# Kernel optimization log

Measured on AMD Instinct MI355X. Metric: run time of the kernel, lower is better.

## Reference

```python
import jax, jax.numpy as jnp
import numpy as np

N = 50000
E = 400000
NFEAT = 256
NHID = 64
HEADS = [4, 4, 4]
NCLASS = 121
NEG_SLOPE = 0.2


def gat_conv(h, W, al, ar, src, dst, H, D):
    # h: [N, F_in], W: [F_in, H*D], al/ar: [H, D]
    feat = (h @ W).reshape(N, H, D)                    # [N, H, D]
    el = jnp.sum(feat * al[None], axis=-1)             # [N, H]
    er = jnp.sum(feat * ar[None], axis=-1)             # [N, H]
    e = jax.nn.leaky_relu(el[src] + er[dst], NEG_SLOPE)  # [E, H]
    # edge softmax over incoming edges of each dst node
    m = jax.ops.segment_max(e, dst, num_segments=N)    # [N, H]
    ex = jnp.exp(e - m[dst])                           # [E, H]
    s = jax.ops.segment_sum(ex, dst, num_segments=N)   # [N, H]
    alpha = ex / s[dst]                                # [E, H]
    msg = alpha[..., None] * feat[src]                 # [E, H, D]
    return jax.ops.segment_sum(msg, dst, num_segments=N)  # [N, H, D]


def setup_inputs() -> dict:
    key = jax.random.key(0)
    ks = jax.random.split(key, 12)
    d = {
        "h": jax.random.normal(ks[0], (N, NFEAT), dtype=jnp.float32),
        "src": jax.random.randint(ks[1], (E,), 0, N),
        "dst": jax.random.randint(ks[2], (E,), 0, N),
        "W1": jax.random.normal(ks[3], (NFEAT, HEADS[0] * NHID), dtype=jnp.float32) * 0.05,
        "al1": jax.random.normal(ks[4], (HEADS[0], NHID), dtype=jnp.float32) * 0.1,
        "ar1": jax.random.normal(ks[5], (HEADS[0], NHID), dtype=jnp.float32) * 0.1,
        "W2": jax.random.normal(ks[6], (HEADS[0] * NHID, HEADS[1] * NHID), dtype=jnp.float32) * 0.05,
        "al2": jax.random.normal(ks[7], (HEADS[1], NHID), dtype=jnp.float32) * 0.1,
        "ar2": jax.random.normal(ks[8], (HEADS[1], NHID), dtype=jnp.float32) * 0.1,
        "W3": jax.random.normal(ks[9], (HEADS[1] * NHID, HEADS[2] * NCLASS), dtype=jnp.float32) * 0.05,
        "al3": jax.random.normal(ks[10], (HEADS[2], NCLASS), dtype=jnp.float32) * 0.1,
        "ar3": jax.random.normal(ks[11], (HEADS[2], NCLASS), dtype=jnp.float32) * 0.1,
    }
    return d


def reference(h, src, dst, W1, al1, ar1, W2, al2, ar2, W3, al3, ar3):
    # layer 1: [N, H0, NHID] -> flatten -> ELU (norm='none', drop=0, residual='none')
    x = gat_conv(h, W1, al1, ar1, src, dst, HEADS[0], NHID).reshape(N, -1)
    x = jax.nn.elu(x)
    # layer 2
    x = gat_conv(x, W2, al2, ar2, src, dst, HEADS[1], NHID).reshape(N, -1)
    x = jax.nn.elu(x)
    # output layer: mean over heads
    x = gat_conv(x, W3, al3, ar3, src, dst, HEADS[2], NCLASS).mean(axis=1)
    return x
```

## Files before the change

kernel.cpp:

```cpp
#include <hip/hip_runtime.h>
#include <cstddef>

#define NN 50000
#define NE 400000
#define NH 4
#define NC 121
#define MAXSLOT 600000

typedef __attribute__((ext_vector_type(8))) short short8;
typedef __attribute__((ext_vector_type(4))) float f32x4;
typedef __attribute__((ext_vector_type(2))) float f32x2;

static __device__ __forceinline__ unsigned short f2bf(float f) {
    unsigned u = __float_as_uint(f);
    u += 0x7fffu + ((u >> 16) & 1u);
    return (unsigned short)(u >> 16);
}
static __device__ __forceinline__ f32x2 bfpair(unsigned u) {
    f32x2 r;
    r.x = __uint_as_float(u << 16);
    r.y = __uint_as_float(u & 0xffff0000u);
    return r;
}
static __device__ __forceinline__ void load_lds16(const unsigned short* g, unsigned short* l) {
    __builtin_amdgcn_global_load_lds(
        (const __attribute__((address_space(1))) unsigned*)g,
        (__attribute__((address_space(3))) unsigned*)l, 16, 0, 0);
}

#define PREP_X    3200000
#define PREP_BT1  (PREP_X + 65536)
#define PREP_BT2  (PREP_BT1 + 65536)
#define PREP_CAT  (PREP_BT2 + 131072)
#define PREP_WV   (PREP_CAT + 2048)
#define PREP_SENT (PREP_WV + 256)
#define PREP_END  (PREP_SENT + NE)
__global__ __launch_bounds__(256) void prep_k(const float* __restrict__ h,
                                              const float* __restrict__ W1,
                                              const float* __restrict__ W2,
                                              const float* __restrict__ W3,
                                              const float* __restrict__ al3,
                                              const float* __restrict__ ar3,
                                              const int* __restrict__ dst,
                                              unsigned short* __restrict__ h_bf,
                                              unsigned short* __restrict__ BT1,
                                              unsigned short* __restrict__ BT2,
                                              unsigned short* __restrict__ BTcat,
                                              float* __restrict__ wl3,
                                              float* __restrict__ wr3,
                                              unsigned short* __restrict__ feat_bf,
                                              float* __restrict__ el,
                                              int* __restrict__ deg) {
    int i = blockIdx.x * blockDim.x + threadIdx.x;
    if (i < PREP_X) {
        float4 v = *(const float4*)&h[(size_t)i * 4];
        ushort4 o;
        o.x = f2bf(v.x); o.y = f2bf(v.y); o.z = f2bf(v.z); o.w = f2bf(v.w);
        *(ushort4*)&h_bf[(size_t)i * 4] = o;
    } else if (i < PREP_BT1) {
        int j = i - PREP_X;
        int n = j >> 8, k = j & 255;
        BT1[j] = f2bf(W1[(size_t)k * 256 + n]);
    } else if (i < PREP_BT2) {
        int j = i - PREP_BT1;
        int n = j >> 8, k = j & 255;
        BT2[j] = f2bf(W2[(size_t)k * 256 + n]);
    } else if (i < PREP_CAT) {
        int j = i - PREP_BT2;
        int c = j >> 10, kk = j & 1023;
        int hh = kk >> 8, k = kk & 255;
        float v = (c < NC) ? 0.25f * W3[(size_t)k * 484 + hh * NC + c] : 0.f;
        BTcat[j] = f2bf(v);
    } else if (i < PREP_WV) {
        int j = (i - PREP_CAT) & 1023;
        int sel = (i - PREP_CAT) >> 10;
        int hh = j >> 8, k = j & 255;
        const float* a = sel ? ar3 : al3;
        const float* wrow = W3 + (size_t)k * 484 + hh * NC;
        const float* arow = a + hh * NC;
        float s = 0.f;
        for (int d = 0; d < NC; ++d) s += wrow[d] * arow[d];
        if (sel) wr3[j] = s; else wl3[j] = s;
    } else if (i < PREP_SENT) {
        int j = i - PREP_WV;
        feat_bf[(size_t)NN * 256 + j] = 0;
        if (j < 4) el[NN * 4 + j] = -1e30f;
    } else if (i < PREP_END) {
        atomicAdd(&deg[dst[i - PREP_SENT]], 1);
    }
}

__global__ __launch_bounds__(512) void gemm256(const unsigned short* __restrict__ A,
                                               const unsigned short* __restrict__ BT,
                                               unsigned short* __restrict__ Cb,
                                               const float* __restrict__ al,
                                               const float* __restrict__ ar,
                                               float* __restrict__ el,
                                               float* __restrict__ er,
                                               int M) {
    const int K = 256;
    __shared__ __align__(16) unsigned short Alds[128 * 32];
    __shared__ __align__(16) unsigned short Blds[256 * 32];
    const int tid = threadIdx.x;
    const int wave = tid >> 6;
    const int lane = tid & 63;
    const int quad = lane >> 4;
    const int ml = lane & 15;
    const int m0 = blockIdx.x * 128;
    const int wm0 = (wave >> 2) * 64;
    const int wn0 = (wave & 3) * 64;

    const unsigned short* Ab = A + (size_t)(m0 + wave * 16 + (lane >> 2)) * K + (lane & 3) * 8;
    const unsigned short* Bb = BT + (size_t)(wave * 16 + (lane >> 2)) * K + (lane & 3) * 8;
    unsigned short* AldsW = Alds + wave * 512;
    unsigned short* BldsW = Blds + wave * 512;

    f32x4 acc[4][4] = {};

    for (int k0 = 0; k0 < K; k0 += 32) {
        load_lds16(Ab + k0, AldsW);
        #pragma unroll
        for (int p = 0; p < 2; ++p)
            load_lds16(Bb + (size_t)(p * 128) * K + k0, BldsW + p * 4096);
        __syncthreads();

        short8 af[4], bf[4];
        #pragma unroll
        for (int i = 0; i < 4; ++i)
            af[i] = *(const short8*)&Alds[(wm0 + i * 16 + ml) * 32 + quad * 8];
        #pragma unroll
        for (int j = 0; j < 4; ++j)
            bf[j] = *(const short8*)&Blds[(wn0 + j * 16 + ml) * 32 + quad * 8];
        #pragma unroll
        for (int i = 0; i < 4; ++i)
            #pragma unroll
            for (int j = 0; j < 4; ++j)
                acc[i][j] = __builtin_amdgcn_mfma_f32_16x16x32_bf16(af[i], bf[j], acc[i][j], 0, 0, 0);
        __syncthreads();
    }

    #pragma unroll
    for (int i = 0; i < 4; ++i) {
        #pragma unroll
        for (int reg = 0; reg < 4; ++reg) {
            int m = m0 + wm0 + i * 16 + quad * 4 + reg;
            if (m >= M) continue;
            #pragma unroll
            for (int j = 0; j < 4; ++j) {
                int n = wn0 + j * 16 + ml;
                Cb[(size_t)m * 256 + n] = f2bf(acc[i][j][reg]);
            }
        }
    }

    {
        int head = wave & 3;
        float alv[4], arv[4];
        #pragma unroll
        for (int j = 0; j < 4; ++j) {
            alv[j] = al[head * 64 + j * 16 + ml];
            arv[j] = ar[head * 64 + j * 16 + ml];
        }
        #pragma unroll
        for (int i = 0; i < 4; ++i) {
            #pragma unroll
            for (int reg = 0; reg < 4; ++reg) {
                float sl = 0.f, sr = 0.f;
                #pragma unroll
                for (int j = 0; j < 4; ++j) {
                    float v = acc[i][j][reg];
                    sl += v * alv[j];
                    sr += v * arv[j];
                }
                #pragma unroll
                for (int off = 1; off < 16; off <<= 1) {
                    sl += __shfl_xor(sl, off);
                    sr += __shfl_xor(sr, off);
                }
                int m = m0 + wm0 + i * 16 + quad * 4 + reg;
                if (ml == 0 && m < M) {
                    el[m * 4 + head] = sl;
                    er[m * 4 + head] = sr;
                }
            }
        }
    }
}

__global__ __launch_bounds__(256) void gemm_bf16(const unsigned short* __restrict__ A,
                                                 const unsigned short* __restrict__ BT,
                                                 float* __restrict__ Cf,
                                                 int M, int Nout, int K) {
    __shared__ __align__(16) unsigned short Alds[128 * 32];
    __shared__ __align__(16) unsigned short Blds[128 * 32];
    const int tid = threadIdx.x;
    const int wave = tid >> 6;
    const int lane = tid & 63;
    const int quad = lane >> 4;
    const int ml = lane & 15;
    const int m0 = blockIdx.x * 128;
    const int n0 = blockIdx.y * 128;
    const int wm0 = (wave >> 1) * 64;
    const int wn0 = (wave & 1) * 64;

    const unsigned short* Ab = A + (size_t)(m0 + wave * 16 + (lane >> 2)) * K + (lane & 3) * 8;
    const unsigned short* Bb = BT + (size_t)(n0 + wave * 16 + (lane >> 2)) * K + (lane & 3) * 8;
    unsigned short* AldsW = Alds + wave * 512;
    unsigned short* BldsW = Blds + wave * 512;

    f32x4 acc[4][4] = {};

    for (int k0 = 0; k0 < K; k0 += 32) {
        #pragma unroll
        for (int p = 0; p < 2; ++p) {
            load_lds16(Ab + (size_t)(p * 64) * K + k0, AldsW + p * 2048);
            load_lds16(Bb + (size_t)(p * 64) * K + k0, BldsW + p * 2048);
        }
        __syncthreads();

        short8 af[4], bf[4];
        #pragma unroll
        for (int i = 0; i < 4; ++i)
            af[i] = *(const short8*)&Alds[(wm0 + i * 16 + ml) * 32 + quad * 8];
        #pragma unroll
        for (int j = 0; j < 4; ++j)
            bf[j] = *(const short8*)&Blds[(wn0 + j * 16 + ml) * 32 + quad * 8];
        #pragma unroll
        for (int i = 0; i < 4; ++i)
            #pragma unroll
            for (int j = 0; j < 4; ++j)
                acc[i][j] = __builtin_amdgcn_mfma_f32_16x16x32_bf16(af[i], bf[j], acc[i][j], 0, 0, 0);
        __syncthreads();
    }

    #pragma unroll
    for (int i = 0; i < 4; ++i) {
        #pragma unroll
        for (int reg = 0; reg < 4; ++reg) {
            int m = m0 + wm0 + i * 16 + quad * 4 + reg;
            if (m >= M) continue;
            #pragma unroll
            for (int j = 0; j < 4; ++j) {
                int n = n0 + wn0 + j * 16 + ml;
                if (n < Nout) Cf[(size_t)m * Nout + n] = acc[i][j][reg];
            }
        }
    }
}

__global__ __launch_bounds__(256) void rowptr_k(const int* __restrict__ deg,
                                                int* __restrict__ rowptr,
                                                int* __restrict__ gtotal,
                                                int* __restrict__ ssrc,
                                                int* __restrict__ sdst) {
    __shared__ int sh[256];
    __shared__ int base;
    int i = blockIdx.x * 256 + threadIdx.x;
    int d = (i < NN) ? deg[i] : 0;
    int v = (d + 3) & ~3;
    sh[threadIdx.x] = v;
    __syncthreads();
    for (int off = 1; off < 256; off <<= 1) {
        int t = (threadIdx.x >= off) ? sh[threadIdx.x - off] : 0;
        __syncthreads();
        sh[threadIdx.x] += t;
        __syncthreads();
    }
    if (threadIdx.x == 255) base = atomicAdd(gtotal, sh[255]);
    __syncthreads();
    if (i < NN) {
        int rp = base + sh[threadIdx.x] - v;
        rowptr[i] = rp;
        for (int p = d; p < v; ++p) {
            ssrc[rp + p] = NN << 9;
            sdst[rp + p] = -1;
        }
    }
}

__global__ __launch_bounds__(256) void scatter_k(const int* __restrict__ src,
                                                 const int* __restrict__ dst,
                                                 const int* __restrict__ rowptr,
                                                 int* __restrict__ cursor,
                                                 int* __restrict__ ssrc,
                                                 int* __restrict__ sdst) {
    int e = blockIdx.x * blockDim.x + threadIdx.x;
    if (e >= NE) return;
    int d = dst[e];
    int p = atomicAdd(&cursor[d], 1);
    int pos = rowptr[d] + p;
    ssrc[pos] = src[e] << 9;
    sdst[pos] = d;
}

__global__ __launch_bounds__(256) void edgew_k(const int* __restrict__ ssrc,
                                               const int* __restrict__ sdst,
                                               const int* __restrict__ gtotal,
                                               const float* __restrict__ el,
                                               const float* __restrict__ er,
                                               float* __restrict__ wcsr) {
    int i = blockIdx.x * blockDim.x + threadIdx.x;
    if (i >= gtotal[0]) return;
    int d = sdst[i];
    float w0 = 0.f, w1 = 0.f, w2 = 0.f, w3 = 0.f;
    if (d >= 0) {
        int su = ssrc[i];
        float4 e_l = *(const float4*)((const char*)el + (su >> 5));
        float4 e_r = *(const float4*)&er[d * 4];
        float v0 = e_l.x + e_r.x; v0 = fmaxf(v0, 0.2f * v0);
        float v1 = e_l.y + e_r.y; v1 = fmaxf(v1, 0.2f * v1);
        float v2 = e_l.z + e_r.z; v2 = fmaxf(v2, 0.2f * v2);
        float v3 = e_l.w + e_r.w; v3 = fmaxf(v3, 0.2f * v3);
        w0 = __expf(v0); w1 = __expf(v1); w2 = __expf(v2); w3 = __expf(v3);
    }
    wcsr[0 * MAXSLOT + i] = w0;
    wcsr[1 * MAXSLOT + i] = w1;
    wcsr[2 * MAXSLOT + i] = w2;
    wcsr[3 * MAXSLOT + i] = w3;
}

__global__ __launch_bounds__(256) void agg256(const int* __restrict__ rowptr,
                                              const int* __restrict__ deg,
                                              const int* __restrict__ ssrc,
                                              const float* __restrict__ el,
                                              const float* __restrict__ er,
                                              const unsigned short* __restrict__ feat,
                                              unsigned short* __restrict__ ybf,
                                              const float* __restrict__ wl3,
                                              const float* __restrict__ wr3,
                                              float* __restrict__ el3,
                                              float* __restrict__ er3) {
    int wid = (blockIdx.x * blockDim.x + threadIdx.x) >> 6;
    int lane = threadIdx.x & 63;
    if (wid >= NN) return;
    int n = wid;
    int start = rowptr[n];
    int cnt4 = (deg[n] + 3) & ~3;
    int head = lane >> 4;
    float ern = er[n * 4 + head];
    const char* elb = (const char*)el + head * 4;
    const char* fbase = (const char*)feat + lane * 8;
    f32x2 a01 = {0.f, 0.f}, a23 = {0.f, 0.f};
    float ssum = 0.f;
    for (int k = 0; k < cnt4; k += 4) {
        int4 sv = *(const int4*)&ssrc[start + k];
        float e0 = *(const float*)(elb + (sv.x >> 5));
        float e1 = *(const float*)(elb + (sv.y >> 5));
        float e2 = *(const float*)(elb + (sv.z >> 5));
        float e3 = *(const float*)(elb + (sv.w >> 5));
        float v0 = e0 + ern; v0 = fmaxf(v0, 0.2f * v0); float w0 = __expf(v0);
        float v1 = e1 + ern; v1 = fmaxf(v1, 0.2f * v1); float w1 = __expf(v1);
        float v2 = e2 + ern; v2 = fmaxf(v2, 0.2f * v2); float w2 = __expf(v2);
        float v3 = e3 + ern; v3 = fmaxf(v3, 0.2f * v3); float w3 = __expf(v3);
        uint2 u0 = *(const uint2*)(fbase + sv.x);
        uint2 u1 = *(const uint2*)(fbase + sv.y);
        uint2 u2 = *(const uint2*)(fbase + sv.z);
        uint2 u3 = *(const uint2*)(fbase + sv.w);
        ssum += (w0 + w1) + (w2 + w3);
        a01 += w0 * bfpair(u0.x); a23 += w0 * bfpair(u0.y);
        a01 += w1 * bfpair(u1.x); a23 += w1 * bfpair(u1.y);
        a01 += w2 * bfpair(u2.x); a23 += w2 * bfpair(u2.y);
        a01 += w3 * bfpair(u3.x); a23 += w3 * bfpair(u3.y);
    }
    float inv = ssum > 0.f ? 1.0f / ssum : 0.f;
    float r0 = a01.x * inv, r1 = a01.y * inv, r2 = a23.x * inv, r3 = a23.y * inv;
    r0 = r0 > 0.f ? r0 : (__expf(r0) - 1.f);
    r1 = r1 > 0.f ? r1 : (__expf(r1) - 1.f);
    r2 = r2 > 0.f ? r2 : (__expf(r2) - 1.f);
    r3 = r3 > 0.f ? r3 : (__expf(r3) - 1.f);
    ushort4 o;
    o.x = f2bf(r0); o.y = f2bf(r1); o.z = f2bf(r2); o.w = f2bf(r3);
    *(ushort4*)&ybf[(size_t)n * 256 + lane * 4] = o;

    if (wl3) {
        float sl[4], sr[4];
        #pragma unroll
        for (int h = 0; h < 4; ++h) {
            float4 a4 = *(const float4*)&wl3[h * 256 + lane * 4];
            float4 b4 = *(const float4*)&wr3[h * 256 + lane * 4];
            sl[h] = r0 * a4.x + r1 * a4.y + r2 * a4.z + r3 * a4.w;
            sr[h] = r0 * b4.x + r1 * b4.y + r2 * b4.z + r3 * b4.w;
        }
        #pragma unroll
        for (int off = 32; off; off >>= 1) {
            #pragma unroll
            for (int h = 0; h < 4; ++h) {
                sl[h] += __shfl_xor(sl[h], off);
                sr[h] += __shfl_xor(sr[h], off);
            }
        }
        if (lane == 0) {
            #pragma unroll
            for (int h = 0; h < 4; ++h) {
                el3[n * 4 + h] = sl[h];
                er3[n * 4 + h] = sr[h];
            }
        }
    }
}

__global__ __launch_bounds__(256) void agg3(const int* __restrict__ rowptr,
                                            const int* __restrict__ deg,
                                            const int* __restrict__ ssrc,
                                            const float* __restrict__ wcsr,
                                            const unsigned short* __restrict__ x,
                                            unsigned short* __restrict__ xagg) {
    int wid = (blockIdx.x * blockDim.x + threadIdx.x) >> 6;
    int lane = threadIdx.x & 63;
    if (wid >= NN) return;
    int n = wid;
    int start = rowptr[n];
    int cnt4 = (deg[n] + 3) & ~3;
    const char* xbase = (const char*)x + lane * 8;
    f32x2 accA[4] = {}, accB[4] = {};
    float ssum[4] = {};
    for (int k = 0; k < cnt4; k += 4) {
        int4 sv = *(const int4*)&ssrc[start + k];
        float4 w0 = *(const float4*)&wcsr[0 * MAXSLOT + start + k];
        float4 w1 = *(const float4*)&wcsr[1 * MAXSLOT + start + k];
        float4 w2 = *(const float4*)&wcsr[2 * MAXSLOT + start + k];
        float4 w3 = *(const float4*)&wcsr[3 * MAXSLOT + start + k];
        uint2 u0 = *(const uint2*)(xbase + sv.x);
        uint2 u1 = *(const uint2*)(xbase + sv.y);
        uint2 u2 = *(const uint2*)(xbase + sv.z);
        uint2 u3 = *(const uint2*)(xbase + sv.w);
        ssum[0] += (w0.x + w0.y) + (w0.z + w0.w);
        ssum[1] += (w1.x + w1.y) + (w1.z + w1.w);
        ssum[2] += (w2.x + w2.y) + (w2.z + w2.w);
        ssum[3] += (w3.x + w3.y) + (w3.z + w3.w);
        f32x2 fa = bfpair(u0.x), fA = bfpair(u0.y);
        f32x2 fb = bfpair(u1.x), fB = bfpair(u1.y);
        f32x2 fc = bfpair(u2.x), fC = bfpair(u2.y);
        f32x2 fd = bfpair(u3.x), fD = bfpair(u3.y);
        accA[0] += w0.x * fa + w0.y * fb + w0.z * fc + w0.w * fd;
        accB[0] += w0.x * fA + w0.y * fB + w0.z * fC + w0.w * fD;
        accA[1] += w1.x * fa + w1.y * fb + w1.z * fc + w1.w * fd;
        accB[1] += w1.x * fA + w1.y * fB + w1.z * fC + w1.w * fD;
        accA[2] += w2.x * fa + w2.y * fb + w2.z * fc + w2.w * fd;
        accB[2] += w2.x * fA + w2.y * fB + w2.z * fC + w2.w * fD;
        accA[3] += w3.x * fa + w3.y * fb + w3.z * fc + w3.w * fd;
        accB[3] += w3.x * fA + w3.y * fB + w3.z * fC + w3.w * fD;
    }
    #pragma unroll
    for (int h = 0; h < 4; ++h) {
        float inv = ssum[h] > 0.f ? 1.f / ssum[h] : 0.f;
        ushort4 o;
        o.x = f2bf(accA[h].x * inv); o.y = f2bf(accA[h].y * inv);
        o.z = f2bf(accB[h].x * inv); o.w = f2bf(accB[h].y * inv);
        *(ushort4*)&xagg[(size_t)n * 1024 + h * 256 + lane * 4] = o;
    }
}

extern "C" void kernel_launch(void* const* d_in, const int* in_sizes, int n_in,
                              void* d_out, int out_size, void* d_ws, size_t ws_size,
                              hipStream_t stream) {
    const float* h   = (const float*)d_in[0];
    const int*   src = (const int*)d_in[1];
    const int*   dst = (const int*)d_in[2];
    const float* W1  = (const float*)d_in[3];
    const float* al1 = (const float*)d_in[4];
    const float* ar1 = (const float*)d_in[5];
    const float* W2  = (const float*)d_in[6];
    const float* al2 = (const float*)d_in[7];
    const float* ar2 = (const float*)d_in[8];
    const float* W3  = (const float*)d_in[9];
    const float* al3 = (const float*)d_in[10];
    const float* ar3 = (const float*)d_in[11];
    float* out = (float*)d_out;

    float* ws = (float*)d_ws;
    unsigned short* x_bf    = (unsigned short*)ws;
    unsigned short* h_bf    = (unsigned short*)(ws + 6400000);
    unsigned short* feat_bf = (unsigned short*)(ws + 12800000);
    unsigned short* xagg    = (unsigned short*)(ws + 6400000);
    float* el  = ws + 32000000;
    float* er  = ws + 32200064;
    float* wl3 = ws + 32400064;
    float* wr3 = ws + 32401088;
    unsigned short* BT1   = (unsigned short*)(ws + 32402112);
    unsigned short* BT2   = (unsigned short*)(ws + 32434880);
    unsigned short* BTcat = (unsigned short*)(ws + 32467648);
    float* wcsr = ws + 32533184;
    int* ibase  = (int*)(ws + 34933184);
    int* deg      = ibase;
    int* cursor   = ibase + 50000;
    int* gtotal   = ibase + 100000;
    int* rowptr   = ibase + 100256;
    int* ssrc     = ibase + 150256;
    int* sdst     = ibase + 750256;
    float* el2 = ws + 36283440;
    float* er2 = ws + 36483440;

    const int NB = (NN + 255) / 256;
    const int SLOT_BLOCKS = (MAXSLOT + 255) / 256;

    hipMemsetAsync(deg, 0, (2 * NN + 1) * sizeof(int), stream);

    prep_k<<<(PREP_END + 255) / 256, 256, 0, stream>>>(h, W1, W2, W3, al3, ar3, dst,
                                                       h_bf, BT1, BT2, BTcat, wl3, wr3,
                                                       feat_bf, el, deg);

    rowptr_k<<<NB, 256, 0, stream>>>(deg, rowptr, gtotal, ssrc, sdst);
    scatter_k<<<(NE + 255) / 256, 256, 0, stream>>>(src, dst, rowptr, cursor, ssrc, sdst);

    const int GB = (NN + 127) / 128;
    const int WAVE_BLOCKS = (NN * 64 + 255) / 256;

    gemm256<<<GB, 512, 0, stream>>>(h_bf, BT1, feat_bf, al1, ar1, el, er, NN);
    agg256<<<WAVE_BLOCKS, 256, 0, stream>>>(rowptr, deg, ssrc, el, er, feat_bf, x_bf,
                                            nullptr, nullptr, nullptr, nullptr);

    gemm256<<<GB, 512, 0, stream>>>(x_bf, BT2, feat_bf, al2, ar2, el, er, NN);
    agg256<<<WAVE_BLOCKS, 256, 0, stream>>>(rowptr, deg, ssrc, el, er, feat_bf, x_bf,
                                            wl3, wr3, el2, er2);

    edgew_k<<<SLOT_BLOCKS, 256, 0, stream>>>(ssrc, sdst, gtotal, el2, er2, wcsr);
    agg3<<<WAVE_BLOCKS, 256, 0, stream>>>(rowptr, deg, ssrc, wcsr, x_bf, xagg);
    gemm_bf16<<<dim3(GB, 1), 256, 0, stream>>>(xagg, BTcat, out, NN, NC, 1024);
}
```

Baseline: 376.1 us.

## Fuse layer-3 edge weight computation into agg3 via lane-parallel exp and shuffles

Removes the separate edgew_k kernel and the wcsr buffer, along with the sdst array used only to feed it. agg3 now has each lane compute the exp-leaky-relu weight for one incoming edge, using the el2 row of the source and the er2 row of the destination, then broadcasts the weights across the wave with __shfl. This drops one kernel launch and the global write and read-back of the four-head edge weight arrays, plus the sdst writes in rowptr and scatter. In exchange agg3 does more shuffle and ALU work per edge, and el2 padding is now set to -1e30 so padded slots get a weight of zero.

```diff
diff --git a/kernel.cpp b/kernel.cpp
--- a/kernel.cpp
+++ b/kernel.cpp
@@ -5,7 +5,6 @@
 #define NE 400000
 #define NH 4
 #define NC 121
-#define MAXSLOT 600000
 
 typedef __attribute__((ext_vector_type(8))) short short8;
 typedef __attribute__((ext_vector_type(4))) float f32x4;
@@ -50,6 +49,7 @@
                                               float* __restrict__ wr3,
                                               unsigned short* __restrict__ feat_bf,
                                               float* __restrict__ el,
+                                              float* __restrict__ el2,
                                               int* __restrict__ deg) {
     int i = blockIdx.x * blockDim.x + threadIdx.x;
     if (i < PREP_X) {
@@ -84,7 +84,10 @@
     } else if (i < PREP_SENT) {
         int j = i - PREP_WV;
         feat_bf[(size_t)NN * 256 + j] = 0;
-        if (j < 4) el[NN * 4 + j] = -1e30f;
+        if (j < 4) {
+            el[NN * 4 + j]  = -1e30f;
+            el2[NN * 4 + j] = -1e30f;
+        }
     } else if (i < PREP_END) {
         atomicAdd(&deg[dst[i - PREP_SENT]], 1);
     }
@@ -251,8 +254,7 @@
 __global__ __launch_bounds__(256) void rowptr_k(const int* __restrict__ deg,
                                                 int* __restrict__ rowptr,
                                                 int* __restrict__ gtotal,
-                                                int* __restrict__ ssrc,
-                                                int* __restrict__ sdst) {
+                                                int* __restrict__ ssrc) {
     __shared__ int sh[256];
     __shared__ int base;
     int i = blockIdx.x * 256 + threadIdx.x;
@@ -271,10 +273,8 @@
     if (i < NN) {
         int rp = base + sh[threadIdx.x] - v;
         rowptr[i] = rp;
-        for (int p = d; p < v; ++p) {
+        for (int p = d; p < v; ++p)
             ssrc[rp + p] = NN << 9;
-            sdst[rp + p] = -1;
-        }
     }
 }
 
@@ -282,41 +282,12 @@
                                                  const int* __restrict__ dst,
                                                  const int* __restrict__ rowptr,
                                                  int* __restrict__ cursor,
-                                                 int* __restrict__ ssrc,
-                                                 int* __restrict__ sdst) {
+                                                 int* __restrict__ ssrc) {
     int e = blockIdx.x * blockDim.x + threadIdx.x;
     if (e >= NE) return;
     int d = dst[e];
     int p = atomicAdd(&cursor[d], 1);
-    int pos = rowptr[d] + p;
-    ssrc[pos] = src[e] << 9;
-    sdst[pos] = d;
-}
-
-__global__ __launch_bounds__(256) void edgew_k(const int* __restrict__ ssrc,
-                                               const int* __restrict__ sdst,
-                                               const int* __restrict__ gtotal,
-                                               const float* __restrict__ el,
-                                               const float* __restrict__ er,
-                                               float* __restrict__ wcsr) {
-    int i = blockIdx.x * blockDim.x + threadIdx.x;
-    if (i >= gtotal[0]) return;
-    int d = sdst[i];
-    float w0 = 0.f, w1 = 0.f, w2 = 0.f, w3 = 0.f;
-    if (d >= 0) {
-        int su = ssrc[i];
-        float4 e_l = *(const float4*)((const char*)el + (su >> 5));
-        float4 e_r = *(const float4*)&er[d * 4];
-        float v0 = e_l.x + e_r.x; v0 = fmaxf(v0, 0.2f * v0);
-        float v1 = e_l.y + e_r.y; v1 = fmaxf(v1, 0.2f * v1);
-        float v2 = e_l.z + e_r.z; v2 = fmaxf(v2, 0.2f * v2);
-        float v3 = e_l.w + e_r.w; v3 = fmaxf(v3, 0.2f * v3);
-        w0 = __expf(v0); w1 = __expf(v1); w2 = __expf(v2); w3 = __expf(v3);
-    }
-    wcsr[0 * MAXSLOT + i] = w0;
-    wcsr[1 * MAXSLOT + i] = w1;
-    wcsr[2 * MAXSLOT + i] = w2;
-    wcsr[3 * MAXSLOT + i] = w3;
+    ssrc[rowptr[d] + p] = src[e] << 9;
 }
 
 __global__ __launch_bounds__(256) void agg256(const int* __restrict__ rowptr,
@@ -402,7 +373,8 @@
 __global__ __launch_bounds__(256) void agg3(const int* __restrict__ rowptr,
                                             const int* __restrict__ deg,
                                             const int* __restrict__ ssrc,
-                                            const float* __restrict__ wcsr,
+                                            const float* __restrict__ el,
+                                            const float* __restrict__ er,
                                             const unsigned short* __restrict__ x,
                                             unsigned short* __restrict__ xagg) {
     int wid = (blockIdx.x * blockDim.x + threadIdx.x) >> 6;
@@ -412,34 +384,54 @@
     int start = rowptr[n];
     int cnt4 = (deg[n] + 3) & ~3;
     const char* xbase = (const char*)x + lane * 8;
+    float4 ern = *(const float4*)&er[n * 4];
     f32x2 accA[4] = {}, accB[4] = {};
     float ssum[4] = {};
-    for (int k = 0; k < cnt4; k += 4) {
-        int4 sv = *(const int4*)&ssrc[start + k];
-        float4 w0 = *(const float4*)&wcsr[0 * MAXSLOT + start + k];
-        float4 w1 = *(const float4*)&wcsr[1 * MAXSLOT + start + k];
-        float4 w2 = *(const float4*)&wcsr[2 * MAXSLOT + start + k];
-        float4 w3 = *(const float4*)&wcsr[3 * MAXSLOT + start + k];
-        uint2 u0 = *(const uint2*)(xbase + sv.x);
-        uint2 u1 = *(const uint2*)(xbase + sv.y);
-        uint2 u2 = *(const uint2*)(xbase + sv.z);
-        uint2 u3 = *(const uint2*)(xbase + sv.w);
-        ssum[0] += (w0.x + w0.y) + (w0.z + w0.w);
-        ssum[1] += (w1.x + w1.y) + (w1.z + w1.w);
-        ssum[2] += (w2.x + w2.y) + (w2.z + w2.w);
-        ssum[3] += (w3.x + w3.y) + (w3.z + w3.w);
-        f32x2 fa = bfpair(u0.x), fA = bfpair(u0.y);
-        f32x2 fb = bfpair(u1.x), fB = bfpair(u1.y);
-        f32x2 fc = bfpair(u2.x), fC = bfpair(u2.y);
-        f32x2 fd = bfpair(u3.x), fD = bfpair(u3.y);
-        accA[0] += w0.x * fa + w0.y * fb + w0.z * fc + w0.w * fd;
-        accB[0] += w0.x * fA + w0.y * fB + w0.z * fC + w0.w * fD;
-        accA[1] += w1.x * fa + w1.y * fb + w1.z * fc + w1.w * fd;
-        accB[1] += w1.x * fA + w1.y * fB + w1.z * fC + w1.w * fD;
-        accA[2] += w2.x * fa + w2.y * fb + w2.z * fc + w2.w * fd;
-        accB[2] += w2.x * fA + w2.y * fB + w2.z * fC + w2.w * fD;
-        accA[3] += w3.x * fa + w3.y * fb + w3.z * fc + w3.w * fd;
-        accB[3] += w3.x * fA + w3.y * fB + w3.z * fC + w3.w * fD;
+    for (int base = 0; base < cnt4; base += 64) {
+        float4 w4 = {0.f, 0.f, 0.f, 0.f};
+        int idx = base + lane;
+        if (idx < cnt4) {
+            int su = ssrc[start + idx];
+            float4 e4 = *(const float4*)((const char*)el + (su >> 5));
+            float v0 = e4.x + ern.x; v0 = fmaxf(v0, 0.2f * v0); w4.x = __expf(v0);
+            float v1 = e4.y + ern.y; v1 = fmaxf(v1, 0.2f * v1); w4.y = __expf(v1);
+            float v2 = e4.z + ern.z; v2 = fmaxf(v2, 0.2f * v2); w4.z = __expf(v2);
+            float v3 = e4.w + ern.w; v3 = fmaxf(v3, 0.2f * v3); w4.w = __expf(v3);
+        }
+        int rem = cnt4 - base;
+        int kend = rem > 64 ? 64 : rem;
+        for (int k = 0; k < kend; k += 4) {
+            int4 sv = *(const int4*)&ssrc[start + base + k];
+            float4 wE0, wE1, wE2, wE3;
+            wE0.x = __shfl(w4.x, k);     wE0.y = __shfl(w4.y, k);
+            wE0.z = __shfl(w4.z, k);     wE0.w = __shfl(w4.w, k);
+            wE1.x = __shfl(w4.x, k + 1); wE1.y = __shfl(w4.y, k + 1);
+            wE1.z = __shfl(w4.z, k + 1); wE1.w = __shfl(w4.w, k + 1);
+            wE2.x = __shfl(w4.x, k + 2); wE2.y = __shfl(w4.y, k + 2);
+            wE2.z = __shfl(w4.z, k + 2); wE2.w = __shfl(w4.w, k + 2);
+            wE3.x = __shfl(w4.x, k + 3); wE3.y = __shfl(w4.y, k + 3);
+            wE3.z = __shfl(w4.z, k + 3); wE3.w = __shfl(w4.w, k + 3);
+            uint2 u0 = *(const uint2*)(xbase + sv.x);
+            uint2 u1 = *(const uint2*)(xbase + sv.y);
+            uint2 u2 = *(const uint2*)(xbase + sv.z);
+            uint2 u3 = *(const uint2*)(xbase + sv.w);
+            ssum[0] += (wE0.x + wE1.x) + (wE2.x + wE3.x);
+            ssum[1] += (wE0.y + wE1.y) + (wE2.y + wE3.y);
+            ssum[2] += (wE0.z + wE1.z) + (wE2.z + wE3.z);
+            ssum[3] += (wE0.w + wE1.w) + (wE2.w + wE3.w);
+            f32x2 fa = bfpair(u0.x), fA = bfpair(u0.y);
+            f32x2 fb = bfpair(u1.x), fB = bfpair(u1.y);
+            f32x2 fc = bfpair(u2.x), fC = bfpair(u2.y);
+            f32x2 fd = bfpair(u3.x), fD = bfpair(u3.y);
+            accA[0] += wE0.x * fa + wE1.x * fb + wE2.x * fc + wE3.x * fd;
+            accB[0] += wE0.x * fA + wE1.x * fB + wE2.x * fC + wE3.x * fD;
+            accA[1] += wE0.y * fa + wE1.y * fb + wE2.y * fc + wE3.y * fd;
+            accB[1] += wE0.y * fA + wE1.y * fB + wE2.y * fC + wE3.y * fD;
+            accA[2] += wE0.z * fa + wE1.z * fb + wE2.z * fc + wE3.z * fd;
+            accB[2] += wE0.z * fA + wE1.z * fB + wE2.z * fC + wE3.z * fD;
+            accA[3] += wE0.w * fa + wE1.w * fb + wE2.w * fc + wE3.w * fd;
+            accB[3] += wE0.w * fA + wE1.w * fB + wE2.w * fC + wE3.w * fD;
+        }
     }
     #pragma unroll
     for (int h = 0; h < 4; ++h) {
@@ -480,28 +472,25 @@
     unsigned short* BT1   = (unsigned short*)(ws + 32402112);
     unsigned short* BT2   = (unsigned short*)(ws + 32434880);
     unsigned short* BTcat = (unsigned short*)(ws + 32467648);
-    float* wcsr = ws + 32533184;
-    int* ibase  = (int*)(ws + 34933184);
+    int* ibase  = (int*)(ws + 32533184);
     int* deg      = ibase;
     int* cursor   = ibase + 50000;
     int* gtotal   = ibase + 100000;
     int* rowptr   = ibase + 100256;
     int* ssrc     = ibase + 150256;
-    int* sdst     = ibase + 750256;
-    float* el2 = ws + 36283440;
-    float* er2 = ws + 36483440;
+    float* el2 = ws + 33283440;
+    float* er2 = ws + 33483504;
 
     const int NB = (NN + 255) / 256;
-    const int SLOT_BLOCKS = (MAXSLOT + 255) / 256;
 
     hipMemsetAsync(deg, 0, (2 * NN + 1) * sizeof(int), stream);
 
     prep_k<<<(PREP_END + 255) / 256, 256, 0, stream>>>(h, W1, W2, W3, al3, ar3, dst,
                                                        h_bf, BT1, BT2, BTcat, wl3, wr3,
-                                                       feat_bf, el, deg);
-
-    rowptr_k<<<NB, 256, 0, stream>>>(deg, rowptr, gtotal, ssrc, sdst);
-    scatter_k<<<(NE + 255) / 256, 256, 0, stream>>>(src, dst, rowptr, cursor, ssrc, sdst);
+                                                       feat_bf, el, el2, deg);
+
+    rowptr_k<<<NB, 256, 0, stream>>>(deg, rowptr, gtotal, ssrc);
+    scatter_k<<<(NE + 255) / 256, 256, 0, stream>>>(src, dst, rowptr, cursor, ssrc);
 
     const int GB = (NN + 127) / 128;
     const int WAVE_BLOCKS = (NN * 64 + 255) / 256;
@@ -514,7 +503,6 @@
     agg256<<<WAVE_BLOCKS, 256, 0, stream>>>(rowptr, deg, ssrc, el, er, feat_bf, x_bf,
                                             wl3, wr3, el2, er2);
 
-    edgew_k<<<SLOT_BLOCKS, 256, 0, stream>>>(ssrc, sdst, gtotal, el2, er2, wcsr);
-    agg3<<<WAVE_BLOCKS, 256, 0, stream>>>(rowptr, deg, ssrc, wcsr, x_bf, xagg);
+    agg3<<<WAVE_BLOCKS, 256, 0, stream>>>(rowptr, deg, ssrc, el2, er2, x_bf, xagg);
     gemm_bf16<<<dim3(GB, 1), 256, 0, stream>>>(xagg, BTcat, out, NN, NC, 1024);
 }
```

New measurement: 370.7 us. No clear change (-1.4%).
